# Kernel optimization log

Hardware: AMD Instinct MI355X
Metric: run time of the kernel (lower is better)

The kernel has to match this reference:

```python
import jax, jax.numpy as jnp
import numpy as np

IN_DIM = 8192   # input feature dim (kernel rows)
OUT_DIM = 8192  # output_sz (kernel cols, number of LIF neurons)
INIT_TAU = 2.0  # learnable tau logit; leak = sigmoid(INIT_TAU)
V_TH = 1.0      # v_threshold


def setup_inputs() -> dict:
    key = jax.random.key(0)
    k1, k2 = jax.random.split(key, 2)
    x = jax.random.normal(k1, (IN_DIM,), jnp.float32)
    W = jax.random.normal(k2, (IN_DIM, OUT_DIM), jnp.float32) / np.float32(np.sqrt(IN_DIM))
    b = jnp.zeros((OUT_DIM,), jnp.float32)
    u = jnp.zeros((OUT_DIM,), jnp.float32)       # membrane potential carry
    a_hat = jnp.zeros((IN_DIM,), jnp.float32)    # presynaptic eligibility trace carry
    return {"W": W, "b": b, "u": u, "a_hat": a_hat, "x": x}


def reference(W, b, u, a_hat, x):
    # One OTTT step: dense projection + leaky-integrate-fire + spike + trace update.
    sig_tau = jax.nn.sigmoid(INIT_TAU)
    u_pre = sig_tau * u + x @ W + b          # leaky integrate
    s = (u_pre >= V_TH).astype(W.dtype)      # spike (heaviside)
    u_new = u_pre - s * V_TH                 # soft reset
    a_hat_new = sig_tau * a_hat + x          # online eligibility trace: a_hat = sig_tau*a_hat + inputs
    return s, u_new, a_hat_new
```

## Files before the change

kernel.cpp:

```cpp
#include <hip/hip_runtime.h>


#define IN_DIM     8192
#define OUT_DIM    8192
#define SIG_TAU    0.8807970779778823f
#define V_TH       1.0f
#define CHUNK_ROWS 32
#define NCHUNKS    (IN_DIM / CHUNK_ROWS)

__global__ __launch_bounds__(256, 4) void gemv_partial_u32(
    const float* __restrict__ W,
    const float* __restrict__ x,
    float* __restrict__ part)
{
    const int col4 = blockIdx.x * 256 + threadIdx.x;
    const int row0 = blockIdx.y * CHUNK_ROWS;

    __shared__ float xs[CHUNK_ROWS];
    if (threadIdx.x < CHUNK_ROWS) xs[threadIdx.x] = x[row0 + threadIdx.x];
    __syncthreads();

    const float4* Wp = (const float4*)W + (size_t)row0 * (OUT_DIM / 4) + col4;
    float4 acc = make_float4(0.f, 0.f, 0.f, 0.f);

    #pragma unroll
    for (int r = 0; r < CHUNK_ROWS; ++r) {
        float4 w = Wp[(size_t)r * (OUT_DIM / 4)];
        const float xv = xs[r];
        acc.x = fmaf(xv, w.x, acc.x);
        acc.y = fmaf(xv, w.y, acc.y);
        acc.z = fmaf(xv, w.z, acc.z);
        acc.w = fmaf(xv, w.w, acc.w);
    }

    ((float4*)part)[(size_t)blockIdx.y * (OUT_DIM / 4) + col4] = acc;
}

__global__ __launch_bounds__(256) void gemv_partial_gen(
    const float* __restrict__ W,
    const float* __restrict__ x,
    float* __restrict__ part,
    int chunk_rows)
{
    const int col4 = blockIdx.x * 256 + threadIdx.x;
    const int row0 = blockIdx.y * chunk_rows;

    extern __shared__ float xsg[];
    for (int t = threadIdx.x; t < chunk_rows; t += 256)
        xsg[t] = x[row0 + t];
    __syncthreads();

    const float4* Wp = (const float4*)W + (size_t)row0 * (OUT_DIM / 4) + col4;
    float4 acc = make_float4(0.f, 0.f, 0.f, 0.f);

    #pragma unroll 8
    for (int r = 0; r < chunk_rows; ++r) {
        float4 w = Wp[(size_t)r * (OUT_DIM / 4)];
        const float xv = xsg[r];
        acc.x = fmaf(xv, w.x, acc.x);
        acc.y = fmaf(xv, w.y, acc.y);
        acc.z = fmaf(xv, w.z, acc.z);
        acc.w = fmaf(xv, w.w, acc.w);
    }

    ((float4*)part)[(size_t)blockIdx.y * (OUT_DIM / 4) + col4] = acc;
}

__global__ __launch_bounds__(256) void finalize_lif(
    const float* __restrict__ part,
    const float* __restrict__ b,
    const float* __restrict__ u,
    const float* __restrict__ a_hat,
    const float* __restrict__ x,
    float* __restrict__ out,
    int nchunks)
{
    const int j = blockIdx.x * 256 + threadIdx.x;
    if (j >= OUT_DIM) return;

    float sum = 0.f;
    #pragma unroll 8
    for (int c = 0; c < nchunks; ++c)
        sum += part[(size_t)c * OUT_DIM + j];

    const float u_pre = fmaf(SIG_TAU, u[j], sum + b[j]);
    const float s = (u_pre >= V_TH) ? 1.0f : 0.0f;

    out[j]               = s;
    out[OUT_DIM + j]     = u_pre - s * V_TH;
    out[2 * OUT_DIM + j] = fmaf(SIG_TAU, a_hat[j], x[j]);
}

extern "C" void kernel_launch(void* const* d_in, const int* in_sizes, int n_in,
                              void* d_out, int out_size, void* d_ws, size_t ws_size,
                              hipStream_t stream)
{
    const float* W     = (const float*)d_in[0];
    const float* b     = (const float*)d_in[1];
    const float* u     = (const float*)d_in[2];
    const float* a_hat = (const float*)d_in[3];
    const float* x     = (const float*)d_in[4];
    float* out  = (float*)d_out;
    float* part = (float*)d_ws;

    if ((size_t)NCHUNKS * OUT_DIM * sizeof(float) <= ws_size) {
        dim3 grid(OUT_DIM / (4 * 256), NCHUNKS);
        gemv_partial_u32<<<grid, 256, 0, stream>>>(W, x, part);
        finalize_lif<<<OUT_DIM / 256, 256, 0, stream>>>(part, b, u, a_hat, x, out, NCHUNKS);
    } else {
        int nchunks = 128;
        while (nchunks > 1 && (size_t)nchunks * OUT_DIM * sizeof(float) > ws_size)
            nchunks >>= 1;
        const int chunk_rows = IN_DIM / nchunks;
        dim3 grid(OUT_DIM / (4 * 256), nchunks);
        gemv_partial_gen<<<grid, 256, chunk_rows * sizeof(float), stream>>>(W, x, part, chunk_rows);
        finalize_lif<<<OUT_DIM / 256, 256, 0, stream>>>(part, b, u, a_hat, x, out, nchunks);
    }
}
```

Before: 377.9 us.

## Fuse GEMV and LIF update into a single kernel with in-block reduction

Measured after the change: 347.6 us. 1.09x faster.

```diff
diff --git a/kernel.cpp b/kernel.cpp
--- a/kernel.cpp
+++ b/kernel.cpp
@@ -1,94 +1,114 @@
 #include <hip/hip_runtime.h>
 
 
-#define IN_DIM     8192
-#define OUT_DIM    8192
-#define SIG_TAU    0.8807970779778823f
-#define V_TH       1.0f
-#define CHUNK_ROWS 32
-#define NCHUNKS    (IN_DIM / CHUNK_ROWS)
+#define IN_DIM   8192
+#define OUT_DIM  8192
+#define SIG_TAU  0.8807970779778823f
+#define V_TH     1.0f
 
-__global__ __launch_bounds__(256, 4) void gemv_partial_u32(
+#define BLK_THREADS  512
+#define FC_PER_BLK   8
+#define ROW_GROUPS   (BLK_THREADS / FC_PER_BLK)
+#define ROWS_PER_THR (IN_DIM / ROW_GROUPS)
+#define NBLOCKS      (OUT_DIM / 4 / FC_PER_BLK)
+
+typedef float f4 __attribute__((ext_vector_type(4)));
+
+__global__ __launch_bounds__(BLK_THREADS) void ottt_fused(
     const float* __restrict__ W,
+    const float* __restrict__ b,
+    const float* __restrict__ u,
+    const float* __restrict__ a_hat,
     const float* __restrict__ x,
-    float* __restrict__ part)
+    float* __restrict__ out)
 {
-    const int col4 = blockIdx.x * 256 + threadIdx.x;
-    const int row0 = blockIdx.y * CHUNK_ROWS;
+    __shared__ float xs[IN_DIM];
+    __shared__ f4 red[ROW_GROUPS][FC_PER_BLK];
+    __shared__ f4 red2[8][FC_PER_BLK];
 
-    __shared__ float xs[CHUNK_ROWS];
-    if (threadIdx.x < CHUNK_ROWS) xs[threadIdx.x] = x[row0 + threadIdx.x];
+    f4* xs4 = (f4*)xs;
+    #pragma unroll
+    for (int i = 0; i < IN_DIM / 4 / BLK_THREADS; ++i)
+        xs4[threadIdx.x + i * BLK_THREADS] =
+            ((const f4*)x)[threadIdx.x + i * BLK_THREADS];
     __syncthreads();
 
-    const float4* Wp = (const float4*)W + (size_t)row0 * (OUT_DIM / 4) + col4;
-    float4 acc = make_float4(0.f, 0.f, 0.f, 0.f);
+    const int fc   = threadIdx.x & (FC_PER_BLK - 1);
+    const int rg   = threadIdx.x >> 3;
+    const int c4   = blockIdx.x * FC_PER_BLK + fc;
+    const int row0 = rg * ROWS_PER_THR;
 
-    #pragma unroll
-    for (int r = 0; r < CHUNK_ROWS; ++r) {
-        float4 w = Wp[(size_t)r * (OUT_DIM / 4)];
-        const float xv = xs[r];
+    const f4* Wp = (const f4*)W + (size_t)row0 * (OUT_DIM / 4) + c4;
+    f4 acc = {0.f, 0.f, 0.f, 0.f};
+
+    #pragma unroll 8
+    for (int r = 0; r < ROWS_PER_THR; ++r) {
+        const f4 w = __builtin_nontemporal_load(&Wp[(size_t)r * (OUT_DIM / 4)]);
+        const float xv = xs[row0 + r];
         acc.x = fmaf(xv, w.x, acc.x);
         acc.y = fmaf(xv, w.y, acc.y);
         acc.z = fmaf(xv, w.z, acc.z);
         acc.w = fmaf(xv, w.w, acc.w);
     }
 
-    ((float4*)part)[(size_t)blockIdx.y * (OUT_DIM / 4) + col4] = acc;
-}
-
-__global__ __launch_bounds__(256) void gemv_partial_gen(
-    const float* __restrict__ W,
-    const float* __restrict__ x,
-    float* __restrict__ part,
-    int chunk_rows)
-{
-    const int col4 = blockIdx.x * 256 + threadIdx.x;
-    const int row0 = blockIdx.y * chunk_rows;
-
-    extern __shared__ float xsg[];
-    for (int t = threadIdx.x; t < chunk_rows; t += 256)
-        xsg[t] = x[row0 + t];
+    red[rg][fc] = acc;
     __syncthreads();
 
-    const float4* Wp = (const float4*)W + (size_t)row0 * (OUT_DIM / 4) + col4;
-    float4 acc = make_float4(0.f, 0.f, 0.f, 0.f);
+    if (threadIdx.x < 64) {
+        const int f = threadIdx.x & 7;
+        const int g = threadIdx.x >> 3;
+        f4 s = red[g * 8][f];
+        #pragma unroll
+        for (int j = 1; j < 8; ++j) {
+            const f4 r = red[g * 8 + j][f];
+            s.x += r.x; s.y += r.y; s.z += r.z; s.w += r.w;
+        }
+        red2[g][f] = s;
+    }
+    __syncthreads();
 
-    #pragma unroll 8
-    for (int r = 0; r < chunk_rows; ++r) {
-        float4 w = Wp[(size_t)r * (OUT_DIM / 4)];
-        const float xv = xsg[r];
-        acc.x = fmaf(xv, w.x, acc.x);
-        acc.y = fmaf(xv, w.y, acc.y);
-        acc.z = fmaf(xv, w.z, acc.z);
-        acc.w = fmaf(xv, w.w, acc.w);
+    if (threadIdx.x < FC_PER_BLK) {
+        const int c4g = blockIdx.x * FC_PER_BLK + threadIdx.x;
+
+        f4 sum = red2[0][threadIdx.x];
+        #pragma unroll
+        for (int g = 1; g < 8; ++g) {
+            const f4 r = red2[g][threadIdx.x];
+            sum.x += r.x; sum.y += r.y; sum.z += r.z; sum.w += r.w;
+        }
+
+        const f4 b4  = ((const f4*)b)[c4g];
+        const f4 u4  = ((const f4*)u)[c4g];
+        const f4 ah4 = ((const f4*)a_hat)[c4g];
+        const f4 x4  = xs4[c4g];
+
+        f4 s4, un4, an4;
+        {
+            const float up = fmaf(SIG_TAU, u4.x, sum.x + b4.x);
+            s4.x = (up >= V_TH) ? 1.0f : 0.0f; un4.x = up - s4.x * V_TH;
+            an4.x = fmaf(SIG_TAU, ah4.x, x4.x);
+        }
+        {
+            const float up = fmaf(SIG_TAU, u4.y, sum.y + b4.y);
+            s4.y = (up >= V_TH) ? 1.0f : 0.0f; un4.y = up - s4.y * V_TH;
+            an4.y = fmaf(SIG_TAU, ah4.y, x4.y);
+        }
+        {
+            const float up = fmaf(SIG_TAU, u4.z, sum.z + b4.z);
+            s4.z = (up >= V_TH) ? 1.0f : 0.0f; un4.z = up - s4.z * V_TH;
+            an4.z = fmaf(SIG_TAU, ah4.z, x4.z);
+        }
+        {
+            const float up = fmaf(SIG_TAU, u4.w, sum.w + b4.w);
+            s4.w = (up >= V_TH) ? 1.0f : 0.0f; un4.w = up - s4.w * V_TH;
+            an4.w = fmaf(SIG_TAU, ah4.w, x4.w);
+        }
+
+        f4* o = (f4*)out;
+        o[c4g]                     = s4;
+        o[(OUT_DIM / 4) + c4g]     = un4;
+        o[2 * (OUT_DIM / 4) + c4g] = an4;
     }
-
-    ((float4*)part)[(size_t)blockIdx.y * (OUT_DIM / 4) + col4] = acc;
-}
-
-__global__ __launch_bounds__(256) void finalize_lif(
-    const float* __restrict__ part,
-    const float* __restrict__ b,
-    const float* __restrict__ u,
-    const float* __restrict__ a_hat,
-    const float* __restrict__ x,
-    float* __restrict__ out,
-    int nchunks)
-{
-    const int j = blockIdx.x * 256 + threadIdx.x;
-    if (j >= OUT_DIM) return;
-
-    float sum = 0.f;
-    #pragma unroll 8
-    for (int c = 0; c < nchunks; ++c)
-        sum += part[(size_t)c * OUT_DIM + j];
-
-    const float u_pre = fmaf(SIG_TAU, u[j], sum + b[j]);
-    const float s = (u_pre >= V_TH) ? 1.0f : 0.0f;
-
-    out[j]               = s;
-    out[OUT_DIM + j]     = u_pre - s * V_TH;
-    out[2 * OUT_DIM + j] = fmaf(SIG_TAU, a_hat[j], x[j]);
 }
 
 extern "C" void kernel_launch(void* const* d_in, const int* in_sizes, int n_in,
@@ -100,20 +120,9 @@
     const float* u     = (const float*)d_in[2];
     const float* a_hat = (const float*)d_in[3];
     const float* x     = (const float*)d_in[4];
-    float* out  = (float*)d_out;
-    float* part = (float*)d_ws;
+    float* out = (float*)d_out;
 
-    if ((size_t)NCHUNKS * OUT_DIM * sizeof(float) <= ws_size) {
-        dim3 grid(OUT_DIM / (4 * 256), NCHUNKS);
-        gemv_partial_u32<<<grid, 256, 0, stream>>>(W, x, part);
-        finalize_lif<<<OUT_DIM / 256, 256, 0, stream>>>(part, b, u, a_hat, x, out, NCHUNKS);
-    } else {
-        int nchunks = 128;
-        while (nchunks > 1 && (size_t)nchunks * OUT_DIM * sizeof(float) > ws_size)
-            nchunks >>= 1;
-        const int chunk_rows = IN_DIM / nchunks;
-        dim3 grid(OUT_DIM / (4 * 256), nchunks);
-        gemv_partial_gen<<<grid, 256, chunk_rows * sizeof(float), stream>>>(W, x, part, chunk_rows);
-        finalize_lif<<<OUT_DIM / 256, 256, 0, stream>>>(part, b, u, a_hat, x, out, nchunks);
-    }
+    (void)d_ws; (void)ws_size;
+
+    ottt_fused<<<NBLOCKS, BLK_THREADS, 0, stream>>>(W, b, u, a_hat, x, out);
 }
```
